# Optimization experiments

Measured on AMD Instinct MI355X. Metric: run time of the kernel, lower is better.

Reference implementation:

```python
import jax, jax.numpy as jnp
import numpy as np

DIM = 1024
NUM_HEADS = 16
HEAD_DIM = DIM // NUM_HEADS

def setup_inputs() -> dict:
    key = jax.random.key(0)
    ks = jax.random.split(key, 5)
    s = 1.0 / np.sqrt(DIM)
    x = jax.random.normal(ks[0], (2, 2048, DIM), dtype=jnp.float32)
    W_qkv = jax.random.uniform(ks[1], (DIM, 3 * DIM), dtype=jnp.float32, minval=-s, maxval=s)
    b_qkv = jax.random.uniform(ks[2], (3 * DIM,), dtype=jnp.float32, minval=-s, maxval=s)
    W_out = jax.random.uniform(ks[3], (DIM, DIM), dtype=jnp.float32, minval=-s, maxval=s)
    b_out = jax.random.uniform(ks[4], (DIM,), dtype=jnp.float32, minval=-s, maxval=s)
    return {"x": x, "W_qkv": W_qkv, "b_qkv": b_qkv, "W_out": W_out, "b_out": b_out}

def reference(x, W_qkv, b_qkv, W_out, b_out):
    B, S, _ = x.shape
    qkv = x @ W_qkv + b_qkv                       # [B,S,3*dim]
    q, k, v = jnp.split(qkv, 3, axis=-1)
    # [B,S,dim] -> [B,H,S,hd]
    def to_heads(t):
        return t.reshape(B, S, NUM_HEADS, HEAD_DIM).transpose(0, 2, 1, 3)
    q, k, v = to_heads(q), to_heads(k), to_heads(v)
    scale = HEAD_DIM ** -0.5
    scores = jnp.einsum('bhqd,bhkd->bhqk', q, k) * scale
    attn = jax.nn.softmax(scores, axis=-1)
    out = jnp.einsum('bhqk,bhkd->bhqd', attn, v)  # [B,H,S,hd]
    out = out.transpose(0, 2, 1, 3).reshape(B, S, DIM)
    return out @ W_out + b_out
```

## Files before the change

kernel.cpp:

```cpp
#include <hip/hip_runtime.h>
#include <math.h>

#define DIMM    1024
#define NHEADS  16
#define HDIM    64
#define BATCH   2
#define SEQ     2048
#define ROWS    (BATCH*SEQ)

typedef _Float16 f16x8 __attribute__((ext_vector_type(8)));
typedef _Float16 f16x4 __attribute__((ext_vector_type(4)));
typedef _Float16 h2    __attribute__((ext_vector_type(2)));
typedef float    f32x4 __attribute__((ext_vector_type(4)));
typedef float    f32x16 __attribute__((ext_vector_type(16)));

__device__ inline void gl_lds16(const void* g, void* l) {
    __builtin_amdgcn_global_load_lds(
        (const __attribute__((address_space(1))) void*)g,
        (__attribute__((address_space(3))) void*)l, 16, 0, 0);
}

static __device__ inline f16x8 mkfrag(unsigned a, unsigned b, unsigned c, unsigned d) {
    union { unsigned u[4]; f16x8 v; } x;
    x.u[0] = a; x.u[1] = b; x.u[2] = c; x.u[3] = d;
    return x.v;
}
static __device__ inline f16x8 cvt8(const float4& a, const float4& b) {
    unsigned u0 = __builtin_bit_cast(unsigned, __builtin_amdgcn_cvt_pkrtz(a.x, a.y));
    unsigned u1 = __builtin_bit_cast(unsigned, __builtin_amdgcn_cvt_pkrtz(a.z, a.w));
    unsigned u2 = __builtin_bit_cast(unsigned, __builtin_amdgcn_cvt_pkrtz(b.x, b.y));
    unsigned u3 = __builtin_bit_cast(unsigned, __builtin_amdgcn_cvt_pkrtz(b.z, b.w));
    return mkfrag(u0, u1, u2, u3);
}

__device__ void tcvt64(const float* __restrict__ in, _Float16* __restrict__ out,
                       int K, int N, int k0, int n0, float (*tile)[65], int t)
{
    {
        const int c4 = (t & 15) * 4;
        const int r  = t >> 4;
        #pragma unroll
        for (int i = 0; i < 4; i++) {
            const int rr = r + 16 * i;
            float4 v = *(const float4*)(in + (size_t)(k0 + rr) * N + n0 + c4);
            tile[rr][c4] = v.x; tile[rr][c4 + 1] = v.y;
            tile[rr][c4 + 2] = v.z; tile[rr][c4 + 3] = v.w;
        }
    }
    __syncthreads();
    #pragma unroll
    for (int i = 0; i < 2; i++) {
        const int seg = t + 256 * i;
        const int n   = seg >> 3;
        const int kc  = (seg & 7) * 8;
        f16x8 o;
        #pragma unroll
        for (int j = 0; j < 8; j++) o[j] = (_Float16)tile[kc + j][n];
        *(f16x8*)(out + (size_t)(n0 + n) * K + k0 + kc) = o;
    }
}

__global__ __launch_bounds__(256)
void prep_kernel(const float* __restrict__ Wqkv, const float* __restrict__ Wout,
                 _Float16* __restrict__ wqkvt, _Float16* __restrict__ woutt)
{
    __shared__ float tile[64][65];
    const int bx = blockIdx.x;
    const int t  = threadIdx.x;
    if (bx < 768) {
        const int gx = bx % 48, gy = bx / 48;
        tcvt64(Wqkv, wqkvt, DIMM, 3 * DIMM, gy * 64, gx * 64, tile, t);
    } else {
        const int id = bx - 768;
        const int gx = id & 15, gy = id >> 4;
        tcvt64(Wout, woutt, DIMM, DIMM, gy * 64, gx * 64, tile, t);
    }
}

__global__ __launch_bounds__(512)
void hgemm256_kernel(const float* __restrict__ X, const _Float16* __restrict__ Bt,
                     const float* __restrict__ bias, _Float16* __restrict__ C,
                     _Float16* __restrict__ vtg, int N, int K)
{
    __shared__ __align__(16) _Float16 lds[65536];

    const int t    = threadIdx.x;
    const int w    = t >> 6, lane = t & 63;
    const int l31  = lane & 31;
    const int hf   = lane >> 5;
    const int l7   = lane & 7;
    const int wm   = w >> 2;
    const int wn   = w & 3;
    const int row0 = blockIdx.y * 256, col0 = blockIdx.x * 256;

    f32x16 acc[4][2];
    #pragma unroll
    for (int mi = 0; mi < 4; mi++)
        #pragma unroll
        for (int ni = 0; ni < 2; ni++)
            #pragma unroll
            for (int r = 0; r < 16; r++) acc[mi][ni][r] = 0.f;

    const float*    gAf[4];
    const _Float16* gB[4];
    int sofs[4];
    #pragma unroll
    for (int j = 0; j < 4; j++) {
        const int s   = t + 512 * j;
        const int row = s >> 3;
        const int kb  = (s & 7) ^ (row & 7);
        gAf[j] = X  + (size_t)(row0 + row) * K + kb * 8;
        gB[j]  = Bt + (size_t)(col0 + row) * K + kb * 8;
        sofs[j] = s * 8;
    }

    {
        float4 pa[4], pb[4];
        #pragma unroll
        for (int j = 0; j < 4; j++) {
            pa[j] = *(const float4*)(gAf[j]);
            pb[j] = *(const float4*)(gAf[j] + 4);
        }
        #pragma unroll
        for (int j = 0; j < 4; j++) *(f16x8*)(lds + sofs[j]) = cvt8(pa[j], pb[j]);
        #pragma unroll
        for (int j = 0; j < 4; j++) gl_lds16(gB[j], lds + 32768 + sofs[j]);
        #pragma unroll
        for (int j = 0; j < 4; j++) { gAf[j] += 64; gB[j] += 64; }
    }

    const int niter = K >> 6;
    #pragma unroll 1
    for (int it = 0; it < niter; it++) {
        const int cur = it & 1;
        __syncthreads();

        float4 pa[4], pb[4];
        const int nxt = cur ^ 1;
        if (it + 1 < niter) {
            #pragma unroll
            for (int j = 0; j < 4; j++) {
                pa[j] = *(const float4*)(gAf[j]);
                pb[j] = *(const float4*)(gAf[j] + 4);
            }
            #pragma unroll
            for (int j = 0; j < 4; j++)
                gl_lds16(gB[j], lds + 32768 + nxt * 16384 + sofs[j]);
            #pragma unroll
            for (int j = 0; j < 4; j++) { gAf[j] += 64; gB[j] += 64; }
        }

        const _Float16* AsC = lds + cur * 16384;
        const _Float16* BsC = lds + 32768 + cur * 16384;
        #pragma unroll
        for (int ks = 0; ks < 4; ks++) {
            const int pseg = ((ks * 2 + hf) ^ l7) * 8;
            f16x8 bf0 = *(const f16x8*)(BsC + (wn * 64 +      l31) * 64 + pseg);
            f16x8 bf1 = *(const f16x8*)(BsC + (wn * 64 + 32 + l31) * 64 + pseg);
            #pragma unroll
            for (int mi = 0; mi < 4; mi++) {
                f16x8 af = *(const f16x8*)(AsC + (wm * 128 + mi * 32 + l31) * 64 + pseg);
                acc[mi][0] = __builtin_amdgcn_mfma_f32_32x32x16_f16(af, bf0, acc[mi][0], 0, 0, 0);
                acc[mi][1] = __builtin_amdgcn_mfma_f32_32x32x16_f16(af, bf1, acc[mi][1], 0, 0, 0);
            }
        }

        if (it + 1 < niter) {
            #pragma unroll
            for (int j = 0; j < 4; j++)
                *(f16x8*)(lds + nxt * 16384 + sofs[j]) = cvt8(pa[j], pb[j]);
        }
    }

    float bv[2];
    #pragma unroll
    for (int ni = 0; ni < 2; ni++) bv[ni] = bias[col0 + wn * 64 + ni * 32 + l31];

    if (blockIdx.x < 8) {
        #pragma unroll
        for (int mi = 0; mi < 4; mi++)
            #pragma unroll
            for (int ni = 0; ni < 2; ni++) {
                const int col = col0 + wn * 64 + ni * 32 + l31;
                #pragma unroll
                for (int r = 0; r < 16; r++) {
                    const int row = row0 + wm * 128 + mi * 32 + (r & 3) + 8 * (r >> 2) + 4 * hf;
                    C[(size_t)row * N + col] = (_Float16)(acc[mi][ni][r] + bv[ni]);
                }
            }
        return;
    }

    __syncthreads();
    #pragma unroll
    for (int mi = 0; mi < 4; mi++)
        #pragma unroll
        for (int ni = 0; ni < 2; ni++) {
            const int coll = wn * 64 + ni * 32 + l31;
            #pragma unroll
            for (int rq = 0; rq < 4; rq++) {
                f16x4 o;
                #pragma unroll
                for (int ri = 0; ri < 4; ri++) o[ri] = (_Float16)(acc[mi][ni][rq * 4 + ri] + bv[ni]);
                const int sidx = rq + 4 * mi + 16 * wm;
                *(f16x4*)(lds + coll * 256 + ((sidx ^ (coll & 31)) << 3) + 4 * hf) = o;
            }
        }
    __syncthreads();
    {
        const int cl   = t >> 1;
        const int half = t & 1;
        const int head = ((blockIdx.x - 8) << 2) + (cl >> 6);
        const int dv   = cl & 63;
        const int bb   = blockIdx.y >> 3;
        const int key0 = (blockIdx.y & 7) * 256 + half * 128;
        _Float16* dst = vtg + ((size_t)(bb * 16 + head) * 64 + dv) * SEQ + key0;
        #pragma unroll
        for (int c = 0; c < 16; c++) {
            const int cs = half * 16 + c;
            *(f16x8*)(dst + c * 8) = *(const f16x8*)(lds + cl * 256 + ((cs ^ (cl & 31)) << 3));
        }
    }
}

__global__ __launch_bounds__(256)
void hgemm_out_kernel(const _Float16* __restrict__ A, const _Float16* __restrict__ Bt,
                      const float* __restrict__ bias, float* __restrict__ Cout,
                      int N, int K)
{
    constexpr int BM = 64, MI = 2;
    __shared__ _Float16 As[2][BM * 64];
    __shared__ _Float16 Bs[2][128 * 64];

    const int t    = threadIdx.x;
    const int w    = t >> 6, lane = t & 63;
    const int quad = lane >> 4, l16 = lane & 15;
    const int wr   = w >> 1, wc = w & 1;
    const int row0 = blockIdx.y * BM, col0 = blockIdx.x * 128;
    const int sw   = l16 & 7;

    f32x4 acc[MI][4];
    #pragma unroll
    for (int i = 0; i < MI; i++)
        #pragma unroll
        for (int j = 0; j < 4; j++)
            #pragma unroll
            for (int r = 0; r < 4; r++) acc[i][j][r] = 0.f;

    const _Float16* gA[MI];
    int aofs[MI];
    #pragma unroll
    for (int j = 0; j < MI; j++) {
        const int s   = t + 256 * j;
        const int row = s >> 3;
        const int kb  = (s & 7) ^ (row & 7);
        gA[j] = A + (size_t)(row0 + row) * K + kb * 8;
        aofs[j] = s * 8;
    }
    const _Float16* gB[4];
    int bofs[4];
    #pragma unroll
    for (int j = 0; j < 4; j++) {
        const int s   = t + 256 * j;
        const int row = s >> 3;
        const int kb  = (s & 7) ^ (row & 7);
        gB[j] = Bt + (size_t)(col0 + row) * K + kb * 8;
        bofs[j] = s * 8;
    }

    #pragma unroll
    for (int j = 0; j < MI; j++) gl_lds16(gA[j], &As[0][aofs[j]]);
    #pragma unroll
    for (int j = 0; j < 4; j++)  gl_lds16(gB[j], &Bs[0][bofs[j]]);
    #pragma unroll
    for (int j = 0; j < MI; j++) gA[j] += 64;
    #pragma unroll
    for (int j = 0; j < 4; j++)  gB[j] += 64;

    const int niter = K >> 6;
    #pragma unroll 1
    for (int it = 0; it < niter; it++) {
        const int cur = it & 1;
        __syncthreads();

        if (it + 1 < niter) {
            const int nxt = cur ^ 1;
            #pragma unroll
            for (int j = 0; j < MI; j++) gl_lds16(gA[j], &As[nxt][aofs[j]]);
            #pragma unroll
            for (int j = 0; j < 4; j++)  gl_lds16(gB[j], &Bs[nxt][bofs[j]]);
            #pragma unroll
            for (int j = 0; j < MI; j++) gA[j] += 64;
            #pragma unroll
            for (int j = 0; j < 4; j++)  gB[j] += 64;
        }

        const _Float16* AsC = &As[cur][0];
        const _Float16* BsC = &Bs[cur][0];
        f16x8 af[MI][2], bf[4][2];
        #pragma unroll
        for (int i = 0; i < MI; i++) {
            const int arow = wr * (BM / 2) + i * 16 + l16;
            #pragma unroll
            for (int hh = 0; hh < 2; hh++)
                af[i][hh] = *(const f16x8*)(AsC + (arow * 8 + ((hh * 4 + quad) ^ sw)) * 8);
        }
        #pragma unroll
        for (int j = 0; j < 4; j++) {
            const int brow = wc * 64 + j * 16 + l16;
            #pragma unroll
            for (int hh = 0; hh < 2; hh++)
                bf[j][hh] = *(const f16x8*)(BsC + (brow * 8 + ((hh * 4 + quad) ^ sw)) * 8);
        }
        #pragma unroll
        for (int i = 0; i < MI; i++)
            #pragma unroll
            for (int j = 0; j < 4; j++) {
                acc[i][j] = __builtin_amdgcn_mfma_f32_16x16x32_f16(af[i][0], bf[j][0], acc[i][j], 0, 0, 0);
                acc[i][j] = __builtin_amdgcn_mfma_f32_16x16x32_f16(af[i][1], bf[j][1], acc[i][j], 0, 0, 0);
            }
    }

    #pragma unroll
    for (int j = 0; j < 4; j++) {
        const int col = col0 + wc * 64 + j * 16 + l16;
        const float bv = bias[col];
        #pragma unroll
        for (int i = 0; i < MI; i++) {
            const int row = row0 + wr * (BM / 2) + i * 16 + quad * 4;
            #pragma unroll
            for (int r = 0; r < 4; r++)
                Cout[(size_t)(row + r) * N + col] = acc[i][j][r] + bv;
        }
    }
}

__global__ __launch_bounds__(256, 4)
void flash_attn_kernel(const _Float16* __restrict__ qkv,
                       const _Float16* __restrict__ vtg,
                       _Float16* __restrict__ out)
{
    const int lin = blockIdx.y * 32 + blockIdx.x;
    const int bh  = (lin & 7) * 4 + (lin >> 8);
    const int qt  = (lin >> 3) & 31;
    const int b  = bh >> 4, hd = bh & 15;
    const int t    = threadIdx.x;
    const int w    = t >> 6;
    const int lane = t & 63;
    const int qg   = w >> 1;
    const int kh   = w & 1;
    const int l31  = lane & 31;
    const int hf   = lane >> 5;
    const int l7   = lane & 7;

    __shared__ __align__(16) _Float16 Ks [2][64 * 64];
    __shared__ __align__(16) _Float16 Vts[2][64 * 64];

    const int q0 = qt * 64;
    const size_t rstr = 3 * DIMM;
    const _Float16* qbase = qkv + (size_t)b * SEQ * rstr;

    f16x8 qf[4];
    {
        const _Float16* qrow = qbase + (size_t)(q0 + qg * 32 + l31) * rstr + hd * HDIM;
        #pragma unroll
        for (int dd = 0; dd < 4; dd++)
            qf[dd] = *(const f16x8*)(qrow + dd * 16 + hf * 8);
    }

    f32x16 Oacc[2];
    #pragma unroll
    for (int dh = 0; dh < 2; dh++)
        #pragma unroll
        for (int r = 0; r < 16; r++) Oacc[dh][r] = 0.f;
    float lrow = 0.f;
    const h2 k1 = {(_Float16)1.f, (_Float16)1.f};

    const int seg0 = t, seg1 = t + 256;
    const int r0 = seg0 >> 3, lb0 = (seg0 & 7) ^ (r0 & 7);
    const int r1 = seg1 >> 3, lb1 = (seg1 & 7) ^ (r1 & 7);
    const _Float16* gK0 = qbase + (size_t)r0 * rstr + DIMM + hd * HDIM + lb0 * 8;
    const _Float16* gK1 = qbase + (size_t)r1 * rstr + DIMM + hd * HDIM + lb1 * 8;
    const _Float16* gV0 = vtg + ((size_t)bh * 64 + r0) * SEQ + lb0 * 8;
    const _Float16* gV1 = vtg + ((size_t)bh * 64 + r1) * SEQ + lb1 * 8;

    gl_lds16(gK0, &Ks [0][seg0 * 8]);
    gl_lds16(gK1, &Ks [0][seg1 * 8]);
    gl_lds16(gV0, &Vts[0][seg0 * 8]);
    gl_lds16(gV1, &Vts[0][seg1 * 8]);

    #pragma unroll 2
    for (int k0 = 0; k0 < SEQ; k0 += 64) {
        const int cur = (k0 >> 6) & 1;
        const _Float16* KsC  = &Ks [cur][0];
        const _Float16* VtsC = &Vts[cur][0];

        __syncthreads();

        f32x16 sacc;
        #pragma unroll
        for (int r = 0; r < 16; r++) sacc[r] = 0.f;
        __builtin_amdgcn_s_setprio(1);
        #pragma unroll
        for (int dd = 0; dd < 4; dd++) {
            f16x8 kf = *(const f16x8*)(KsC + (kh * 32 + l31) * 64 + (((dd * 2 + hf) ^ l7) * 8));
            sacc = __builtin_amdgcn_mfma_f32_32x32x16_f16(kf, qf[dd], sacc, 0, 0, 0);
        }
        __builtin_amdgcn_s_setprio(0);

        if (k0 + 64 < SEQ) {
            const int nxt = cur ^ 1;
            gl_lds16(gK0 + (size_t)(k0 + 64) * rstr, &Ks [nxt][seg0 * 8]);
            gl_lds16(gK1 + (size_t)(k0 + 64) * rstr, &Ks [nxt][seg1 * 8]);
            gl_lds16(gV0 + (k0 + 64),                &Vts[nxt][seg0 * 8]);
            gl_lds16(gV1 + (k0 + 64),                &Vts[nxt][seg1 * 8]);
        }

        float e[16];
        #pragma unroll
        for (int r = 0; r < 16; r++) {
            const float xx = sacc[r] * 0.18033688011112042f;
            float ee;
            asm("v_exp_f32 %0, %1" : "=v"(ee) : "v"(xx));
            e[r] = ee;
        }

        unsigned w01 = __builtin_bit_cast(unsigned, __builtin_amdgcn_cvt_pkrtz(e[0],  e[1]));
        unsigned w23 = __builtin_bit_cast(unsigned, __builtin_amdgcn_cvt_pkrtz(e[2],  e[3]));
        unsigned w45 = __builtin_bit_cast(unsigned, __builtin_amdgcn_cvt_pkrtz(e[4],  e[5]));
        unsigned w67 = __builtin_bit_cast(unsigned, __builtin_amdgcn_cvt_pkrtz(e[6],  e[7]));
        unsigned w89 = __builtin_bit_cast(unsigned, __builtin_amdgcn_cvt_pkrtz(e[8],  e[9]));
        unsigned wab = __builtin_bit_cast(unsigned, __builtin_amdgcn_cvt_pkrtz(e[10], e[11]));
        unsigned wcd = __builtin_bit_cast(unsigned, __builtin_amdgcn_cvt_pkrtz(e[12], e[13]));
        unsigned wef = __builtin_bit_cast(unsigned, __builtin_amdgcn_cvt_pkrtz(e[14], e[15]));

        lrow = __builtin_amdgcn_fdot2(__builtin_bit_cast(h2, w01), k1, lrow, false);
        lrow = __builtin_amdgcn_fdot2(__builtin_bit_cast(h2, w23), k1, lrow, false);
        lrow = __builtin_amdgcn_fdot2(__builtin_bit_cast(h2, w45), k1, lrow, false);
        lrow = __builtin_amdgcn_fdot2(__builtin_bit_cast(h2, w67), k1, lrow, false);
        lrow = __builtin_amdgcn_fdot2(__builtin_bit_cast(h2, w89), k1, lrow, false);
        lrow = __builtin_amdgcn_fdot2(__builtin_bit_cast(h2, wab), k1, lrow, false);
        lrow = __builtin_amdgcn_fdot2(__builtin_bit_cast(h2, wcd), k1, lrow, false);
        lrow = __builtin_amdgcn_fdot2(__builtin_bit_cast(h2, wef), k1, lrow, false);

        unsigned p00 = w01, p02 = w45;
        asm("v_permlane32_swap_b32 %0, %1" : "+v"(p00), "+v"(p02));
        unsigned p01 = w23, p03 = w67;
        asm("v_permlane32_swap_b32 %0, %1" : "+v"(p01), "+v"(p03));
        unsigned p10 = w89, p12 = wcd;
        asm("v_permlane32_swap_b32 %0, %1" : "+v"(p10), "+v"(p12));
        unsigned p11 = wab, p13 = wef;
        asm("v_permlane32_swap_b32 %0, %1" : "+v"(p11), "+v"(p13));
        f16x8 pa0 = mkfrag(p00, p01, p02, p03);
        f16x8 pa1 = mkfrag(p10, p11, p12, p13);

        __builtin_amdgcn_s_setprio(1);
        #pragma unroll
        for (int dh = 0; dh < 2; dh++) {
            const _Float16* vrow = VtsC + (dh * 32 + l31) * 64;
            f16x8 vf0 = *(const f16x8*)(vrow + (((kh * 4 + 0 + hf) ^ l7) * 8));
            f16x8 vf1 = *(const f16x8*)(vrow + (((kh * 4 + 2 + hf) ^ l7) * 8));
            Oacc[dh] = __builtin_amdgcn_mfma_f32_32x32x16_f16(pa0, vf0, Oacc[dh], 0, 0, 0);
            Oacc[dh] = __builtin_amdgcn_mfma_f32_32x32x16_f16(pa1, vf1, Oacc[dh], 0, 0, 0);
        }
        __builtin_amdgcn_s_setprio(0);
    }

    float lsum = lrow + __shfl_xor(lrow, 32);
    __syncthreads();
    float* Obuf = (float*)&Ks[0][0];
    float* lbuf = (float*)&Vts[0][0];
    if (kh) {
        #pragma unroll
        for (int dh = 0; dh < 2; dh++)
            #pragma unroll
            for (int r = 0; r < 16; r++) {
                const int q = (r & 3) + 8 * (r >> 2) + 4 * hf;
                Obuf[(qg * 32 + q) * 64 + dh * 32 + l31] = Oacc[dh][r];
            }
        if (lane < 32) lbuf[qg * 32 + lane] = lsum;
    }
    __syncthreads();
    if (!kh) {
        const float dnrec = 1.f / (lsum + lbuf[qg * 32 + l31]);
        float dq[16];
        #pragma unroll
        for (int r = 0; r < 16; r++)
            dq[r] = __shfl(dnrec, (r & 3) + 8 * (r >> 2) + 4 * hf);
        #pragma unroll
        for (int dh = 0; dh < 2; dh++)
            #pragma unroll
            for (int r = 0; r < 16; r++) {
                const int q = (r & 3) + 8 * (r >> 2) + 4 * hf;
                const float v = (Oacc[dh][r] + Obuf[(qg * 32 + q) * 64 + dh * 32 + l31])
                                * dq[r];
                out[(size_t)(b * SEQ + q0 + qg * 32 + q) * DIMM + hd * HDIM + dh * 32 + l31] =
                    (_Float16)v;
            }
    }
}

extern "C" void kernel_launch(void* const* d_in, const int* in_sizes, int n_in,
                              void* d_out, int out_size, void* d_ws, size_t ws_size,
                              hipStream_t stream)
{
    const float* x    = (const float*)d_in[0];
    const float* Wqkv = (const float*)d_in[1];
    const float* bqkv = (const float*)d_in[2];
    const float* Wout = (const float*)d_in[3];
    const float* bout = (const float*)d_in[4];
    float* out = (float*)d_out;

    _Float16* qkvh  = (_Float16*)d_ws;
    _Float16* attnh = qkvh  + (size_t)ROWS * 3 * DIMM;
    _Float16* xh    = attnh + (size_t)ROWS * DIMM;
    _Float16* wqkvt = xh    + (size_t)ROWS * DIMM;
    _Float16* woutt = wqkvt + (size_t)3 * DIMM * DIMM;
    _Float16* vtg   = woutt + (size_t)DIMM * DIMM;

    prep_kernel<<<1024, 256, 0, stream>>>(Wqkv, Wout, wqkvt, woutt);
    {
        dim3 grid(3 * DIMM / 256, ROWS / 256);
        hgemm256_kernel<<<grid, 512, 0, stream>>>(x, wqkvt, bqkv, qkvh, vtg, 3 * DIMM, DIMM);
    }
    {
        dim3 grid(SEQ / 64, BATCH * NHEADS);
        flash_attn_kernel<<<grid, 256, 0, stream>>>(qkvh, vtg, attnh);
    }
    {
        dim3 grid(DIMM / 128, ROWS / 64);
        hgemm_out_kernel<<<grid, 256, 0, stream>>>(attnh, woutt, bout, out, DIMM, DIMM);
    }
}
```

Baseline: 187.2 us.

## Retile QKV GEMM to 256x192 blocks to fill all CUs

```diff
diff --git a/kernel.cpp b/kernel.cpp
--- a/kernel.cpp
+++ b/kernel.cpp
@@ -82,36 +82,44 @@
                      const float* __restrict__ bias, _Float16* __restrict__ C,
                      _Float16* __restrict__ vtg, int N, int K)
 {
-    __shared__ __align__(16) _Float16 lds[65536];
+    __shared__ __align__(16) _Float16 lds[57344];
 
     const int t    = threadIdx.x;
     const int w    = t >> 6, lane = t & 63;
     const int l31  = lane & 31;
     const int hf   = lane >> 5;
     const int l7   = lane & 7;
-    const int wm   = w >> 2;
-    const int wn   = w & 3;
-    const int row0 = blockIdx.y * 256, col0 = blockIdx.x * 256;
-
-    f32x16 acc[4][2];
-    #pragma unroll
-    for (int mi = 0; mi < 4; mi++)
-        #pragma unroll
-        for (int ni = 0; ni < 2; ni++)
+    const int wm   = w >> 1;
+    const int wn   = w & 1;
+    const int row0 = blockIdx.y * 256, col0 = blockIdx.x * 192;
+
+    f32x16 acc[2][3];
+    #pragma unroll
+    for (int mi = 0; mi < 2; mi++)
+        #pragma unroll
+        for (int ni = 0; ni < 3; ni++)
             #pragma unroll
             for (int r = 0; r < 16; r++) acc[mi][ni][r] = 0.f;
 
     const float*    gAf[4];
-    const _Float16* gB[4];
-    int sofs[4];
+    int aofs[4];
     #pragma unroll
     for (int j = 0; j < 4; j++) {
         const int s   = t + 512 * j;
         const int row = s >> 3;
         const int kb  = (s & 7) ^ (row & 7);
-        gAf[j] = X  + (size_t)(row0 + row) * K + kb * 8;
-        gB[j]  = Bt + (size_t)(col0 + row) * K + kb * 8;
-        sofs[j] = s * 8;
+        gAf[j] = X + (size_t)(row0 + row) * K + kb * 8;
+        aofs[j] = s * 8;
+    }
+    const _Float16* gB[3];
+    int bofs[3];
+    #pragma unroll
+    for (int j = 0; j < 3; j++) {
+        const int s   = t + 512 * j;
+        const int row = s >> 3;
+        const int kb  = (s & 7) ^ (row & 7);
+        gB[j] = Bt + (size_t)(col0 + row) * K + kb * 8;
+        bofs[j] = s * 8;
     }
 
     {
@@ -122,11 +130,13 @@
             pb[j] = *(const float4*)(gAf[j] + 4);
         }
         #pragma unroll
-        for (int j = 0; j < 4; j++) *(f16x8*)(lds + sofs[j]) = cvt8(pa[j], pb[j]);
-        #pragma unroll
-        for (int j = 0; j < 4; j++) gl_lds16(gB[j], lds + 32768 + sofs[j]);
-        #pragma unroll
-        for (int j = 0; j < 4; j++) { gAf[j] += 64; gB[j] += 64; }
+        for (int j = 0; j < 4; j++) *(f16x8*)(lds + aofs[j]) = cvt8(pa[j], pb[j]);
+        #pragma unroll
+        for (int j = 0; j < 3; j++) gl_lds16(gB[j], lds + 32768 + bofs[j]);
+        #pragma unroll
+        for (int j = 0; j < 4; j++) gAf[j] += 64;
+        #pragma unroll
+        for (int j = 0; j < 3; j++) gB[j] += 64;
     }
 
     const int niter = K >> 6;
@@ -144,81 +154,94 @@
                 pb[j] = *(const float4*)(gAf[j] + 4);
             }
             #pragma unroll
-            for (int j = 0; j < 4; j++)
-                gl_lds16(gB[j], lds + 32768 + nxt * 16384 + sofs[j]);
-            #pragma unroll
-            for (int j = 0; j < 4; j++) { gAf[j] += 64; gB[j] += 64; }
+            for (int j = 0; j < 3; j++)
+                gl_lds16(gB[j], lds + 32768 + nxt * 12288 + bofs[j]);
+            #pragma unroll
+            for (int j = 0; j < 4; j++) gAf[j] += 64;
+            #pragma unroll
+            for (int j = 0; j < 3; j++) gB[j] += 64;
         }
 
         const _Float16* AsC = lds + cur * 16384;
-        const _Float16* BsC = lds + 32768 + cur * 16384;
+        const _Float16* BsC = lds + 32768 + cur * 12288;
         #pragma unroll
         for (int ks = 0; ks < 4; ks++) {
             const int pseg = ((ks * 2 + hf) ^ l7) * 8;
-            f16x8 bf0 = *(const f16x8*)(BsC + (wn * 64 +      l31) * 64 + pseg);
-            f16x8 bf1 = *(const f16x8*)(BsC + (wn * 64 + 32 + l31) * 64 + pseg);
-            #pragma unroll
-            for (int mi = 0; mi < 4; mi++) {
-                f16x8 af = *(const f16x8*)(AsC + (wm * 128 + mi * 32 + l31) * 64 + pseg);
-                acc[mi][0] = __builtin_amdgcn_mfma_f32_32x32x16_f16(af, bf0, acc[mi][0], 0, 0, 0);
-                acc[mi][1] = __builtin_amdgcn_mfma_f32_32x32x16_f16(af, bf1, acc[mi][1], 0, 0, 0);
+            f16x8 bf[3];
+            #pragma unroll
+            for (int ni = 0; ni < 3; ni++)
+                bf[ni] = *(const f16x8*)(BsC + (wn * 96 + ni * 32 + l31) * 64 + pseg);
+            #pragma unroll
+            for (int mi = 0; mi < 2; mi++) {
+                f16x8 af = *(const f16x8*)(AsC + (wm * 64 + mi * 32 + l31) * 64 + pseg);
+                #pragma unroll
+                for (int ni = 0; ni < 3; ni++)
+                    acc[mi][ni] = __builtin_amdgcn_mfma_f32_32x32x16_f16(af, bf[ni], acc[mi][ni], 0, 0, 0);
             }
         }
 
         if (it + 1 < niter) {
             #pragma unroll
             for (int j = 0; j < 4; j++)
-                *(f16x8*)(lds + nxt * 16384 + sofs[j]) = cvt8(pa[j], pb[j]);
-        }
-    }
-
-    float bv[2];
-    #pragma unroll
-    for (int ni = 0; ni < 2; ni++) bv[ni] = bias[col0 + wn * 64 + ni * 32 + l31];
-
-    if (blockIdx.x < 8) {
-        #pragma unroll
-        for (int mi = 0; mi < 4; mi++)
-            #pragma unroll
-            for (int ni = 0; ni < 2; ni++) {
-                const int col = col0 + wn * 64 + ni * 32 + l31;
+                *(f16x8*)(lds + nxt * 16384 + aofs[j]) = cvt8(pa[j], pb[j]);
+        }
+    }
+
+    float bv[3];
+    #pragma unroll
+    for (int ni = 0; ni < 3; ni++) bv[ni] = bias[col0 + wn * 96 + ni * 32 + l31];
+
+    #pragma unroll
+    for (int mi = 0; mi < 2; mi++)
+        #pragma unroll
+        for (int ni = 0; ni < 3; ni++) {
+            const int col = col0 + wn * 96 + ni * 32 + l31;
+            if (col < 2048) {
                 #pragma unroll
                 for (int r = 0; r < 16; r++) {
-                    const int row = row0 + wm * 128 + mi * 32 + (r & 3) + 8 * (r >> 2) + 4 * hf;
+                    const int row = row0 + wm * 64 + mi * 32 + (r & 3) + 8 * (r >> 2) + 4 * hf;
                     C[(size_t)row * N + col] = (_Float16)(acc[mi][ni][r] + bv[ni]);
                 }
             }
-        return;
-    }
+        }
+
+    if (col0 + 192 <= 2048) return;
 
     __syncthreads();
     #pragma unroll
-    for (int mi = 0; mi < 4; mi++)
-        #pragma unroll
-        for (int ni = 0; ni < 2; ni++) {
-            const int coll = wn * 64 + ni * 32 + l31;
-            #pragma unroll
-            for (int rq = 0; rq < 4; rq++) {
-                f16x4 o;
+    for (int mi = 0; mi < 2; mi++)
+        #pragma unroll
+        for (int ni = 0; ni < 3; ni++) {
+            const int coll = wn * 96 + ni * 32 + l31;
+            if (col0 + coll >= 2048) {
                 #pragma unroll
-                for (int ri = 0; ri < 4; ri++) o[ri] = (_Float16)(acc[mi][ni][rq * 4 + ri] + bv[ni]);
-                const int sidx = rq + 4 * mi + 16 * wm;
-                *(f16x4*)(lds + coll * 256 + ((sidx ^ (coll & 31)) << 3) + 4 * hf) = o;
+                for (int rq = 0; rq < 4; rq++) {
+                    f16x4 o;
+                    #pragma unroll
+                    for (int ri = 0; ri < 4; ri++) o[ri] = (_Float16)(acc[mi][ni][rq * 4 + ri] + bv[ni]);
+                    const int sidx = rq + 4 * mi + 8 * wm;
+                    *(f16x4*)(lds + coll * 256 + ((sidx ^ (coll & 31)) << 3) + 4 * hf) = o;
+                }
             }
         }
     __syncthreads();
     {
         const int cl   = t >> 1;
         const int half = t & 1;
-        const int head = ((blockIdx.x - 8) << 2) + (cl >> 6);
-        const int dv   = cl & 63;
-        const int bb   = blockIdx.y >> 3;
-        const int key0 = (blockIdx.y & 7) * 256 + half * 128;
-        _Float16* dst = vtg + ((size_t)(bb * 16 + head) * 64 + dv) * SEQ + key0;
-        #pragma unroll
-        for (int c = 0; c < 16; c++) {
-            const int cs = half * 16 + c;
-            *(f16x8*)(dst + c * 8) = *(const f16x8*)(lds + cl * 256 + ((cs ^ (cl & 31)) << 3));
+        if (cl < 192) {
+            const int col = col0 + cl;
+            if (col >= 2048) {
+                const int head = (col - 2048) >> 6;
+                const int dv   = (col - 2048) & 63;
+                const int bb   = blockIdx.y >> 3;
+                const int key0 = (blockIdx.y & 7) * 256 + half * 128;
+                _Float16* dst = vtg + ((size_t)(bb * 16 + head) * 64 + dv) * SEQ + key0;
+                #pragma unroll
+                for (int c = 0; c < 16; c++) {
+                    const int cs = half * 16 + c;
+                    *(f16x8*)(dst + c * 8) = *(const f16x8*)(lds + cl * 256 + ((cs ^ (cl & 31)) << 3));
+                }
+            }
         }
     }
 }
@@ -520,7 +543,7 @@
 
     prep_kernel<<<1024, 256, 0, stream>>>(Wqkv, Wout, wqkvt, woutt);
     {
-        dim3 grid(3 * DIMM / 256, ROWS / 256);
+        dim3 grid(3 * DIMM / 192, ROWS / 256);
         hgemm256_kernel<<<grid, 512, 0, stream>>>(x, wqkvt, bqkv, qkvh, vtg, 3 * DIMM, DIMM);
     }
     {
```

Measured after the change: 186.7 us. About the same (-0.2%).
